# Performance work log

Measured on AMD Instinct MI355X. Metric: run time of the kernel, lower is better.

Reference implementation:

```python
import jax, jax.numpy as jnp
import numpy as np

N_NODES = 100_000
N_EDGES = 1_600_000
F_DIM = 32


def setup_inputs() -> dict:
    key = jax.random.key(0)
    k1, k2, k3 = jax.random.split(key, 3)
    x = jax.random.normal(k1, (N_NODES, F_DIM), dtype=jnp.float32)
    edge_index = jax.random.randint(k2, (2, N_EDGES), 0, N_NODES, dtype=jnp.int64)
    edge_weight = jax.random.uniform(k3, (N_EDGES,), dtype=jnp.float32)
    w_mp = jnp.array([0.5], dtype=jnp.float32)  # learned scalar parameter
    return {"x": x, "edge_index": edge_index, "edge_weight": edge_weight, "w_mp": w_mp}


def reference(x, edge_index, edge_weight, w_mp):
    # message: ea = w_mp * x[src] * edge_weight  (shape [E, F])
    # aggregate: sum messages into target nodes (aggr='add', source_to_target)
    src = edge_index[0]
    dst = edge_index[1]
    ea = (w_mp * x[src]) * edge_weight[:, None]          # [E, F]
    out = jax.ops.segment_sum(ea, dst, num_segments=x.shape[0])  # [N, F]
    return out
```

## Files before the change

### kernel.cpp

```cpp
#include <hip/hip_runtime.h>


constexpr int N_NODES = 100000;
constexpr int N_EDGES = 1600000;
constexpr int F_DIM   = 32;

constexpr int NPB_C = 256;
constexpr int NB_C  = (N_NODES + NPB_C - 1) / NPB_C;
constexpr int CAP_C = 4608;

constexpr int CUR_STRIDE = 32;

constexpr int BIN_THREADS = 1024;
constexpr int BIN_BLOCKS  = 256;
constexpr int BIN_CHUNK   = N_EDGES / BIN_BLOCKS;
constexpr int BIN_EPT     = (BIN_CHUNK + BIN_THREADS - 1) / BIN_THREADS;

constexpr int AGG_THREADS = 1024;
constexpr int GRPT = (CAP_C + AGG_THREADS - 1) / AGG_THREADS;

constexpr size_t WS_CURSOR  = 0;
constexpr size_t WS_RECORDS = 64 * 1024;
constexpr size_t WS_NEEDED  = WS_RECORDS + (size_t)NB_C * CAP_C * 8;

__global__ __launch_bounds__(BIN_THREADS) void bin_edges(
    const int* __restrict__ src, const int* __restrict__ dst,
    const float* __restrict__ ew, const float* __restrict__ w_mp,
    int* __restrict__ gcursor, uint2* __restrict__ records)
{
    __shared__ int lhist[NB_C];
    __shared__ int lbase[NB_C];
    if (threadIdx.x < NB_C) lhist[threadIdx.x] = 0;
    __syncthreads();

    const float w = w_mp[0];
    const int base_e = blockIdx.x * BIN_CHUNK;
    const int e_end  = min(base_e + BIN_CHUNK, N_EDGES);
    int   bkt[BIN_EPT];
    uint2 rec[BIN_EPT];

    #pragma unroll
    for (int i = 0; i < BIN_EPT; ++i) {
        int e = base_e + threadIdx.x + i * BIN_THREADS;
        bkt[i] = -1;
        if (e < e_end) {
            int d = dst[e];
            int b = d >> 8;
            bkt[i] = b;
            rec[i].x = __float_as_uint(w * ew[e]);
            rec[i].y = (unsigned)src[e] | ((unsigned)(d & 255) << 24);
            atomicAdd(&lhist[b], 1);
        }
    }
    __syncthreads();

    if (threadIdx.x < NB_C) {
        int c = lhist[threadIdx.x];
        int base = c ? atomicAdd(&gcursor[threadIdx.x * CUR_STRIDE], c) : 0;
        lbase[threadIdx.x] = threadIdx.x * CAP_C + base;
        lhist[threadIdx.x] = 0;
    }
    __syncthreads();

    #pragma unroll
    for (int i = 0; i < BIN_EPT; ++i) {
        int b = bkt[i];
        if (b >= 0) {
            int pos = lbase[b] + atomicAdd(&lhist[b], 1);
            if (pos < (b + 1) * CAP_C)
                records[pos] = rec[i];
        }
    }
}

__global__ __launch_bounds__(AGG_THREADS, 8) void sort_gather(
    const int*   __restrict__ gcursor,
    const uint2* __restrict__ records,
    const float* __restrict__ x,
    float*       __restrict__ out)
{
    __shared__ uint2 sorted[CAP_C];
    __shared__ int   hist[NPB_C];
    __shared__ int   offs[NPB_C + 1];
    __shared__ int   cursor[NPB_C];

    const int coarse = blockIdx.x;
    const int t      = threadIdx.x;

    if (t < NPB_C) hist[t] = 0;
    __syncthreads();

    const int rbase = coarse * CAP_C;
    const int cnt   = min(gcursor[coarse * CUR_STRIDE], CAP_C);

    uint2 rec[GRPT];
    #pragma unroll
    for (int i = 0; i < GRPT; ++i) {
        int j = t + i * AGG_THREADS;
        rec[i].y = 0xFFFFFFFFu;
        if (j < cnt) {
            rec[i] = records[rbase + j];
            atomicAdd(&hist[rec[i].y >> 24], 1);
        }
    }
    __syncthreads();

    if (t < 64) {
        const int b4 = t * 4;
        int h0 = hist[b4], h1 = hist[b4 + 1], h2 = hist[b4 + 2], h3 = hist[b4 + 3];
        int s   = h0 + h1 + h2 + h3;
        int inc = s;
        #pragma unroll
        for (int d = 1; d < 64; d <<= 1) {
            int o = __shfl_up(inc, d, 64);
            if (t >= d) inc += o;
        }
        int base = inc - s;
        offs[b4]     = base;
        offs[b4 + 1] = base + h0;
        offs[b4 + 2] = base + h0 + h1;
        offs[b4 + 3] = base + h0 + h1 + h2;
        cursor[b4]     = base;
        cursor[b4 + 1] = base + h0;
        cursor[b4 + 2] = base + h0 + h1;
        cursor[b4 + 3] = base + h0 + h1 + h2;
        if (t == 63) offs[NPB_C] = inc;
    }
    __syncthreads();

    #pragma unroll
    for (int i = 0; i < GRPT; ++i) {
        if (rec[i].y != 0xFFFFFFFFu) {
            int slot = atomicAdd(&cursor[rec[i].y >> 24], 1);
            sorted[slot] = rec[i];
        }
    }
    __syncthreads();

    const int qq = (t & 7) * 4;
    #pragma unroll
    for (int p = 0; p < 2; ++p) {
        const int node  = p * (AGG_THREADS / 8) + (t >> 3);
        const int gnode = coarse * NPB_C + node;
        if (gnode >= N_NODES) continue;

        int j  = offs[node];
        int je = offs[node + 1];
        float4 acc = make_float4(0.f, 0.f, 0.f, 0.f);

        for (; j + 4 <= je; j += 4) {
            uint2 r0 = sorted[j + 0];
            uint2 r1 = sorted[j + 1];
            uint2 r2 = sorted[j + 2];
            uint2 r3 = sorted[j + 3];
            const float4 v0 = *reinterpret_cast<const float4*>(
                x + (size_t)(r0.y & 0xFFFFFFu) * F_DIM + qq);
            const float4 v1 = *reinterpret_cast<const float4*>(
                x + (size_t)(r1.y & 0xFFFFFFu) * F_DIM + qq);
            const float4 v2 = *reinterpret_cast<const float4*>(
                x + (size_t)(r2.y & 0xFFFFFFu) * F_DIM + qq);
            const float4 v3 = *reinterpret_cast<const float4*>(
                x + (size_t)(r3.y & 0xFFFFFFu) * F_DIM + qq);
            float c0 = __uint_as_float(r0.x), c1 = __uint_as_float(r1.x);
            float c2 = __uint_as_float(r2.x), c3 = __uint_as_float(r3.x);
            acc.x += c0 * v0.x + c1 * v1.x + c2 * v2.x + c3 * v3.x;
            acc.y += c0 * v0.y + c1 * v1.y + c2 * v2.y + c3 * v3.y;
            acc.z += c0 * v0.z + c1 * v1.z + c2 * v2.z + c3 * v3.z;
            acc.w += c0 * v0.w + c1 * v1.w + c2 * v2.w + c3 * v3.w;
        }
        for (; j < je; ++j) {
            uint2 r = sorted[j];
            float c = __uint_as_float(r.x);
            const float4 v = *reinterpret_cast<const float4*>(
                x + (size_t)(r.y & 0xFFFFFFu) * F_DIM + qq);
            acc.x += c * v.x;
            acc.y += c * v.y;
            acc.z += c * v.z;
            acc.w += c * v.w;
        }
        *reinterpret_cast<float4*>(out + (size_t)gnode * F_DIM + qq) = acc;
    }
}

__global__ __launch_bounds__(256) void gnn_scatter_atomic(
    const float* __restrict__ x, const int* __restrict__ src,
    const int* __restrict__ dst, const float* __restrict__ ew,
    const float* __restrict__ w_mp, float* __restrict__ out)
{
    const float w = w_mp[0];
    int gid = blockIdx.x * blockDim.x + threadIdx.x;
    int e = gid >> 3;
    int qq = (gid & 7) * 4;
    if (e >= N_EDGES) return;
    int s = src[e];
    int d = dst[e];
    float c = w * ew[e];
    const float4 xv = *reinterpret_cast<const float4*>(x + (size_t)s * F_DIM + qq);
    float* op = out + (size_t)d * F_DIM + qq;
    atomicAdd(op + 0, c * xv.x);
    atomicAdd(op + 1, c * xv.y);
    atomicAdd(op + 2, c * xv.z);
    atomicAdd(op + 3, c * xv.w);
}

extern "C" void kernel_launch(void* const* d_in, const int* in_sizes, int n_in,
                              void* d_out, int out_size, void* d_ws, size_t ws_size,
                              hipStream_t stream) {
    const float* x    = (const float*)d_in[0];
    const int*   ei   = (const int*)d_in[1];
    const float* ew   = (const float*)d_in[2];
    const float* w_mp = (const float*)d_in[3];
    float* out = (float*)d_out;

    const int* src = ei;
    const int* dst = ei + N_EDGES;

    if (ws_size < WS_NEEDED) {
        hipMemsetAsync(d_out, 0, (size_t)out_size * sizeof(float), stream);
        int total = N_EDGES * 8;
        gnn_scatter_atomic<<<(total + 255) / 256, 256, 0, stream>>>(
            x, src, dst, ew, w_mp, out);
        return;
    }

    char* ws = (char*)d_ws;
    int*   gcursor = (int*)(ws + WS_CURSOR);
    uint2* records = (uint2*)(ws + WS_RECORDS);

    hipMemsetAsync(gcursor, 0, NB_C * CUR_STRIDE * sizeof(int), stream);
    bin_edges<<<BIN_BLOCKS, BIN_THREADS, 0, stream>>>(src, dst, ew, w_mp,
                                                      gcursor, records);
    sort_gather<<<NB_C, AGG_THREADS, 0, stream>>>(gcursor, records, x, out);
}
```

Measured before the change: 121.8 us.

## Locally sort binned edges in shared memory before coalesced record writes

The binning kernel now computes a block-wide exclusive scan of the per-bucket histogram, scatters records into a shared-memory staging buffer ordered by bucket, and then writes them out linearly so that consecutive threads store to contiguous global addresses within each bucket. This replaces random scattered 8-byte global stores with mostly coalesced runs. The block count doubles so each block's chunk fits in shared memory, which adds more global cursor atomics and one more scan and barrier phase per block.

```diff
diff --git a/kernel.cpp b/kernel.cpp
--- a/kernel.cpp
+++ b/kernel.cpp
@@ -12,7 +12,7 @@
 constexpr int CUR_STRIDE = 32;
 
 constexpr int BIN_THREADS = 1024;
-constexpr int BIN_BLOCKS  = 256;
+constexpr int BIN_BLOCKS  = 512;
 constexpr int BIN_CHUNK   = N_EDGES / BIN_BLOCKS;
 constexpr int BIN_EPT     = (BIN_CHUNK + BIN_THREADS - 1) / BIN_THREADS;
 
@@ -23,27 +23,40 @@
 constexpr size_t WS_RECORDS = 64 * 1024;
 constexpr size_t WS_NEEDED  = WS_RECORDS + (size_t)NB_C * CAP_C * 8;
 
-__global__ __launch_bounds__(BIN_THREADS) void bin_edges(
+__global__ __launch_bounds__(BIN_THREADS, 8) void bin_edges(
     const int* __restrict__ src, const int* __restrict__ dst,
     const float* __restrict__ ew, const float* __restrict__ w_mp,
     int* __restrict__ gcursor, uint2* __restrict__ records)
 {
+    __shared__ uint2 srt[BIN_CHUNK];
+    __shared__ unsigned short srtb[BIN_CHUNK];
     __shared__ int lhist[NB_C];
+    __shared__ int loff[NB_C];
     __shared__ int lbase[NB_C];
-    if (threadIdx.x < NB_C) lhist[threadIdx.x] = 0;
+    __shared__ int lcur[NB_C];
+    __shared__ int wsum[8];
+    __shared__ int wexc[8];
+
+    const int t    = threadIdx.x;
+    const int lane = t & 63;
+    const int wv   = t >> 6;
+
+    if (t < NB_C) lhist[t] = 0;
     __syncthreads();
 
     const float w = w_mp[0];
-    const int base_e = blockIdx.x * BIN_CHUNK;
-    const int e_end  = min(base_e + BIN_CHUNK, N_EDGES);
+    const int e0    = blockIdx.x * BIN_CHUNK;
+    const int e_end = min(e0 + BIN_CHUNK, N_EDGES);
+    const int cnt   = e_end - e0;
+
     int   bkt[BIN_EPT];
     uint2 rec[BIN_EPT];
-
     #pragma unroll
     for (int i = 0; i < BIN_EPT; ++i) {
-        int e = base_e + threadIdx.x + i * BIN_THREADS;
+        int j = t + i * BIN_THREADS;
         bkt[i] = -1;
-        if (e < e_end) {
+        if (j < cnt) {
+            int e = e0 + j;
             int d = dst[e];
             int b = d >> 8;
             bkt[i] = b;
@@ -54,22 +67,55 @@
     }
     __syncthreads();
 
-    if (threadIdx.x < NB_C) {
-        int c = lhist[threadIdx.x];
-        int base = c ? atomicAdd(&gcursor[threadIdx.x * CUR_STRIDE], c) : 0;
-        lbase[threadIdx.x] = threadIdx.x * CAP_C + base;
-        lhist[threadIdx.x] = 0;
+    if (t < 448) {
+        int v = (t < NB_C) ? lhist[t] : 0;
+        int inc = v;
+        #pragma unroll
+        for (int d = 1; d < 64; d <<= 1) {
+            int o = __shfl_up(inc, d, 64);
+            if (lane >= d) inc += o;
+        }
+        if (lane == 63) wsum[wv] = inc;
+        if (t < NB_C) loff[t] = inc - v;
+    }
+    __syncthreads();
+    if (t < 64) {
+        int v = (t < 7) ? wsum[t] : 0;
+        int inc = v;
+        #pragma unroll
+        for (int d = 1; d < 8; d <<= 1) {
+            int o = __shfl_up(inc, d, 64);
+            if (t >= d) inc += o;
+        }
+        if (t < 7) wexc[t] = inc - v;
+    }
+    __syncthreads();
+
+    if (t < NB_C) {
+        int off = loff[t] + wexc[t >> 6];
+        loff[t] = off;
+        int c = lhist[t];
+        int base = c ? atomicAdd(&gcursor[t * CUR_STRIDE], c) : 0;
+        lbase[t] = t * CAP_C + base - off;
+        lcur[t]  = off;
     }
     __syncthreads();
 
     #pragma unroll
     for (int i = 0; i < BIN_EPT; ++i) {
-        int b = bkt[i];
-        if (b >= 0) {
-            int pos = lbase[b] + atomicAdd(&lhist[b], 1);
-            if (pos < (b + 1) * CAP_C)
-                records[pos] = rec[i];
-        }
+        if (bkt[i] >= 0) {
+            int s = atomicAdd(&lcur[bkt[i]], 1);
+            srt[s]  = rec[i];
+            srtb[s] = (unsigned short)bkt[i];
+        }
+    }
+    __syncthreads();
+
+    for (int j = t; j < cnt; j += BIN_THREADS) {
+        int b   = srtb[j];
+        int pos = lbase[b] + j;
+        if (pos < (b + 1) * CAP_C)
+            records[pos] = srt[j];
     }
 }
 
```

After: 122.4 us. Within noise of the previous version (+0.5%).
